# Optimization experiments

Measured on AMD Instinct MI355X. Metric: run time of the kernel, lower is better.

Reference implementation:

```python
import jax, jax.numpy as jnp
import numpy as np

MARGIN = 0.3
EPS = 1e-6  # torch TripletMarginLoss pairwise_distance eps


def setup_inputs() -> dict:
    key = jax.random.key(0)
    k1, k2 = jax.random.split(key)
    n, d = 8192, 128
    inputs = jax.random.normal(k1, (n, d), dtype=jnp.float32)
    similarity = jax.random.randint(k2, (n, n), 0, 2, dtype=jnp.int32)
    return {"inputs": inputs, "similarity": similarity}


def reference(inputs, similarity):
    # mask[i, j] = True if j is a positive of anchor i
    mask = similarity != 0                      # (n, n) bool
    maskf = mask.astype(inputs.dtype)
    counts = maskf.sum(axis=1, keepdims=True)   # (n, 1), >0 by construction
    # per-anchor center = mean of its positives (masked mean as a GEMM)
    centers = (maskf @ inputs) / counts         # (n, d)
    # dist[i, j] = ||centers[i] - inputs[j]||_2 via the expansion trick
    # (avoids materializing the (n, n, d) difference tensor of the original)
    c2 = jnp.sum(centers * centers, axis=1)[:, None]
    x2 = jnp.sum(inputs * inputs, axis=1)[None, :]
    d2 = c2 + x2 - 2.0 * (centers @ inputs.T)
    dist = jnp.sqrt(jnp.maximum(d2, 0.0))       # (n, n)
    # dist only feeds argmin in the original (indices carry no grad)
    dist = jax.lax.stop_gradient(dist)
    # hard-negative mining: argmin of dist over negatives of each anchor
    neg_idx = jnp.argmin(jnp.where(mask, jnp.inf, dist), axis=1)  # (n,)
    neg_min = inputs[neg_idx]                   # (n, d)
    # TripletMarginLoss(margin=0.3, p=2): anchor=centers, pos=inputs, neg=neg_min
    d_ap = jnp.linalg.norm(centers - inputs + EPS, axis=1)
    d_an = jnp.linalg.norm(centers - neg_min + EPS, axis=1)
    return jnp.mean(jnp.maximum(d_ap - d_an + MARGIN, 0.0))
```

## Files before the change

### kernel.cpp

```cpp
#include <hip/hip_runtime.h>
#include <stdint.h>

#define NN 8192
#define DD 128

typedef float f32x4 __attribute__((ext_vector_type(4)));
typedef short bf16x8 __attribute__((ext_vector_type(8)));

union B8 { uint32_t u[4]; bf16x8 v; };

__device__ inline uint16_t f2bf(float f) {
  uint32_t u = __builtin_bit_cast(uint32_t, f);
  uint32_t r = (u + 0x7FFFu + ((u >> 16) & 1u)) >> 16;
  return (uint16_t)r;
}

__device__ inline f32x4 mfma16(bf16x8 a, bf16x8 b, f32x4 c) {
  return __builtin_amdgcn_mfma_f32_16x16x32_bf16(a, b, c, 0, 0, 0);
}

__global__ __launch_bounds__(256) void k_prep(const float* __restrict__ inp,
                                              uint16_t* __restrict__ inp_bf,
                                              uint16_t* __restrict__ inpT_bf,
                                              float* __restrict__ x2p) {
  __shared__ uint16_t ldsT[128 * 65];
  __shared__ float ldsS[256];
  const int tid = threadIdx.x;
  const int j0 = blockIdx.x * 64;
  const int r = tid >> 2;
  const int dseg = (tid & 3) * 32;
  float ss = 0.f;
#pragma unroll
  for (int it = 0; it < 8; ++it) {
    float4 v = *(const float4*)(inp + (size_t)(j0 + r) * DD + dseg + it * 4);
    ss += v.x * v.x + v.y * v.y + v.z * v.z + v.w * v.w;
    uint16_t b0 = f2bf(v.x), b1 = f2bf(v.y), b2 = f2bf(v.z), b3 = f2bf(v.w);
    *(ushort4*)(inp_bf + (size_t)(j0 + r) * DD + dseg + it * 4) = make_ushort4(b0, b1, b2, b3);
    int d = dseg + it * 4;
    ldsT[(d + 0) * 65 + r] = b0;
    ldsT[(d + 1) * 65 + r] = b1;
    ldsT[(d + 2) * 65 + r] = b2;
    ldsT[(d + 3) * 65 + r] = b3;
  }
  ldsS[tid] = ss;
  __syncthreads();
  if (tid < 64)
    x2p[j0 + tid] = ldsS[tid * 4] + ldsS[tid * 4 + 1] + ldsS[tid * 4 + 2] + ldsS[tid * 4 + 3] + 512.0f;
#pragma unroll
  for (int it = 0; it < 32; ++it) {
    int flat = it * 256 + tid;
    int d = flat >> 6, jl = flat & 63;
    inpT_bf[(size_t)d * NN + j0 + jl] = ldsT[d * 65 + jl];
  }
}

__global__ __launch_bounds__(256) void k_bitgen(const int* __restrict__ sim,
                                                uint32_t* __restrict__ bmT,
                                                uint32_t* __restrict__ counts) {
  __shared__ uint32_t ldsW[64 * 64];
  const int tid = threadIdx.x, lane = tid & 63, w = tid >> 6;
  const int m0 = blockIdx.x * 64;
  const int c0 = blockIdx.y * 2048;
#pragma unroll 1
  for (int rr = 0; rr < 16; ++rr) {
    const int rl = rr * 4 + w;
    const int row = m0 + rl;
    const int* p = sim + (size_t)row * NN + c0 + lane;
    int v[32];
#pragma unroll
    for (int s = 0; s < 32; ++s) v[s] = p[s * 64];
    uint32_t cnt = 0;
#pragma unroll
    for (int s = 0; s < 32; ++s) {
      unsigned long long ball = __ballot(v[s] != 0);
      cnt += (uint32_t)__popcll(ball);
      if ((lane & 31) == 0)
        ldsW[(s * 2 + (lane >> 5)) * 64 + rl] = (uint32_t)(ball >> (lane & 32));
    }
    if (lane == 0) atomicAdd(&counts[row], cnt);
  }
  __syncthreads();
#pragma unroll
  for (int it = 0; it < 16; ++it) {
    int idx = it * 256 + tid;
    int kw = idx >> 6, r = idx & 63;
    bmT[(size_t)((c0 >> 5) + kw) * NN + m0 + r] = ldsW[idx];
  }
}

__global__ __launch_bounds__(256, 4) void k_gemm1(const uint16_t* __restrict__ inpT,
                                                  const uint32_t* __restrict__ bmT,
                                                  float* __restrict__ part) {
  __shared__ __align__(16) uint16_t ldsB[128 * 40];
  __shared__ uint32_t ldsM[64];
  const int tid = threadIdx.x, lane = tid & 63, w = tid >> 6;
  const int col = lane & 15, quad = lane >> 4;
  const int m0 = blockIdx.x * 64;
  const int kb0 = blockIdx.y * 1024;
  const int wm = (w >> 1) * 32, wn = (w & 1) * 64;
  const int dim = tid >> 1, koff = (tid & 1) * 16;
  f32x4 acc[2][4];
  const f32x4 z = {0.f, 0.f, 0.f, 0.f};
#pragma unroll
  for (int r = 0; r < 2; ++r)
#pragma unroll
    for (int c = 0; c < 4; ++c) acc[r][c] = z;

  bf16x8 bpf0 = *(const bf16x8*)(inpT + (size_t)dim * NN + kb0 + koff);
  bf16x8 bpf1 = *(const bf16x8*)(inpT + (size_t)dim * NN + kb0 + koff + 8);
  uint32_t mpf = (tid < 64) ? bmT[(size_t)(kb0 >> 5) * NN + m0 + tid] : 0u;

  for (int ks = 0; ks < 32; ++ks) {
    const int kb = kb0 + ks * 32;
    __syncthreads();
    *(bf16x8*)(ldsB + dim * 40 + koff) = bpf0;
    *(bf16x8*)(ldsB + dim * 40 + koff + 8) = bpf1;
    if (tid < 64) ldsM[tid] = mpf;
    __syncthreads();
    if (ks < 31) {
      bpf0 = *(const bf16x8*)(inpT + (size_t)dim * NN + kb + 32 + koff);
      bpf1 = *(const bf16x8*)(inpT + (size_t)dim * NN + kb + 32 + koff + 8);
      if (tid < 64) mpf = bmT[(size_t)((kb + 32) >> 5) * NN + m0 + tid];
    }
    B8 af[2];
#pragma unroll
    for (int rr = 0; rr < 2; ++rr) {
      uint32_t word = ldsM[wm + rr * 16 + col];
      uint32_t b = (word >> (quad * 8)) & 0xFFu;
      uint32_t s = b * 0x8001u;
#pragma unroll
      for (int p = 0; p < 4; ++p) {
        uint32_t t = (s >> (2 * p)) & 0x10001u;
        af[rr].u[p] = t * 0x3F80u;
      }
    }
#pragma unroll
    for (int cc = 0; cc < 4; ++cc) {
      bf16x8 bfr = *(const bf16x8*)(ldsB + (wn + cc * 16 + col) * 40 + quad * 8);
#pragma unroll
      for (int rr = 0; rr < 2; ++rr) acc[rr][cc] = mfma16(af[rr].v, bfr, acc[rr][cc]);
    }
  }
  float* pp = part + (size_t)blockIdx.y * NN * DD;
#pragma unroll
  for (int rr = 0; rr < 2; ++rr)
#pragma unroll
    for (int cc = 0; cc < 4; ++cc)
#pragma unroll
      for (int g = 0; g < 4; ++g)
        pp[(size_t)(m0 + wm + rr * 16 + quad * 4 + g) * DD + wn + cc * 16 + col] = acc[rr][cc][g];
}

__global__ __launch_bounds__(256) void k_reduce(const float* __restrict__ part,
                                                const uint32_t* __restrict__ counts,
                                                float* __restrict__ centers,
                                                uint16_t* __restrict__ cen_bf) {
  const int gid = blockIdx.x * 256 + threadIdx.x;
  const int idx = gid * 4;
  const int row = idx >> 7;
  const float inv = 1.0f / (float)counts[row];
  float4 v = *(const float4*)(part + idx);
#pragma unroll
  for (int s = 1; s < 8; ++s) {
    float4 u = *(const float4*)(part + (size_t)s * NN * DD + idx);
    v.x += u.x; v.y += u.y; v.z += u.z; v.w += u.w;
  }
  v.x *= inv; v.y *= inv; v.z *= inv; v.w *= inv;
  *(float4*)(centers + idx) = v;
  *(ushort4*)(cen_bf + idx) = make_ushort4(f2bf(v.x), f2bf(v.y), f2bf(v.z), f2bf(v.w));
}

__global__ __launch_bounds__(256, 4) void k_argmin(const uint16_t* __restrict__ cen_bf,
                                                   const uint16_t* __restrict__ inp_bf,
                                                   const uint32_t* __restrict__ bmT,
                                                   const float* __restrict__ x2p,
                                                   uint32_t* __restrict__ negkey) {
  __shared__ __align__(16) uint16_t ldsB[64 * 136];
  __shared__ uint32_t ldsM[128];
  __shared__ float ldsX[64];
  __shared__ uint32_t ldsR[64];
  const int tid = threadIdx.x, lane = tid & 63, w = tid >> 6;
  const int col = lane & 15, quad = lane >> 4;
  const int i0 = blockIdx.x * 64;
  const int jbase = blockIdx.y * 1024;
  const int wi = (w >> 1) * 32, wj = (w & 1) * 32;
  bf16x8 af[2][4];
#pragma unroll
  for (int rr = 0; rr < 2; ++rr)
#pragma unroll
    for (int kk = 0; kk < 4; ++kk)
      af[rr][kk] = *(const bf16x8*)(cen_bf + (size_t)(i0 + wi + rr * 16 + col) * DD + kk * 32 + quad * 8);
  if (tid < 64) ldsR[tid] = 0xFFFFFFFFu;
  uint32_t best[2][4];
#pragma unroll
  for (int rr = 0; rr < 2; ++rr)
#pragma unroll
    for (int g = 0; g < 4; ++g) best[rr][g] = 0xFFFFFFFFu;

  const int jl = tid >> 2, doff = (tid & 3) * 32;
  bf16x8 bpf[4];
#pragma unroll
  for (int it = 0; it < 4; ++it)
    bpf[it] = *(const bf16x8*)(inp_bf + (size_t)(jbase + jl) * DD + doff + it * 8);
  uint32_t mpf = (tid < 128) ? bmT[(size_t)((jbase >> 5) + (tid >> 6)) * NN + i0 + (tid & 63)] : 0u;
  float xpf = (tid >= 128 && tid < 192) ? x2p[jbase + tid - 128] : 0.f;

  for (int js = 0; js < 16; ++js) {
    const int j0 = jbase + js * 64;
    __syncthreads();
#pragma unroll
    for (int it = 0; it < 4; ++it)
      *(bf16x8*)(ldsB + jl * 136 + doff + it * 8) = bpf[it];
    if (tid < 128) ldsM[tid] = mpf;
    else if (tid < 192) ldsX[tid - 128] = xpf;
    __syncthreads();
    if (js < 15) {
#pragma unroll
      for (int it = 0; it < 4; ++it)
        bpf[it] = *(const bf16x8*)(inp_bf + (size_t)(j0 + 64 + jl) * DD + doff + it * 8);
      if (tid < 128) mpf = bmT[(size_t)(((j0 + 64) >> 5) + (tid >> 6)) * NN + i0 + (tid & 63)];
      else if (tid < 192) xpf = x2p[j0 + 64 + tid - 128];
    }
    f32x4 acc[2][2];
    const f32x4 z = {0.f, 0.f, 0.f, 0.f};
    acc[0][0] = z; acc[0][1] = z; acc[1][0] = z; acc[1][1] = z;
#pragma unroll
    for (int kk = 0; kk < 4; ++kk) {
      bf16x8 b0 = *(const bf16x8*)(ldsB + (wj + col) * 136 + kk * 32 + quad * 8);
      bf16x8 b1 = *(const bf16x8*)(ldsB + (wj + 16 + col) * 136 + kk * 32 + quad * 8);
      acc[0][0] = mfma16(af[0][kk], b0, acc[0][0]);
      acc[0][1] = mfma16(af[0][kk], b1, acc[0][1]);
      acc[1][0] = mfma16(af[1][kk], b0, acc[1][0]);
      acc[1][1] = mfma16(af[1][kk], b1, acc[1][1]);
    }
    const uint32_t wsel = (w & 1) * 64;
    uint32_t words[2][4];
#pragma unroll
    for (int rr = 0; rr < 2; ++rr)
#pragma unroll
      for (int g = 0; g < 4; ++g) words[rr][g] = ldsM[wsel + wi + rr * 16 + quad * 4 + g];
#pragma unroll
    for (int cc = 0; cc < 2; ++cc) {
      const int jj = wj + cc * 16 + col;
      const float xq = ldsX[jj];
      const uint32_t jpre = (uint32_t)(j0 + jj);
      const int sh = 31 - (cc * 16 + col);
#pragma unroll
      for (int rr = 0; rr < 2; ++rr)
#pragma unroll
        for (int g = 0; g < 4; ++g) {
          float v = fmaf(-2.0f, acc[rr][cc][g], xq);
          uint32_t u = __builtin_bit_cast(uint32_t, v);
          uint32_t key = (u & 0xFFFFE000u) | jpre;
          key |= (words[rr][g] << sh) & 0x80000000u;
          best[rr][g] = min(best[rr][g], key);
        }
    }
  }
#pragma unroll
  for (int rr = 0; rr < 2; ++rr)
#pragma unroll
    for (int g = 0; g < 4; ++g) {
      uint32_t k = best[rr][g];
#pragma unroll
      for (int d = 1; d < 16; d <<= 1) {
        uint32_t o = (uint32_t)__shfl_xor((int)k, d);
        k = min(k, o);
      }
      if (col == 0) atomicMin(&ldsR[wi + rr * 16 + quad * 4 + g], k);
    }
  __syncthreads();
  if (tid < 64) atomicMin(&negkey[i0 + tid], ldsR[tid]);
}

__global__ __launch_bounds__(256) void k_loss(const float* __restrict__ centers,
                                              const float* __restrict__ inp,
                                              const uint32_t* __restrict__ negkey,
                                              float* __restrict__ out) {
  __shared__ float lds[4];
  const int tid = threadIdx.x, lane = tid & 63, w = tid >> 6;
  float local = 0.f;
#pragma unroll 1
  for (int a = 0; a < 4; ++a) {
    int i = blockIdx.x * 16 + w * 4 + a;
    float2 c = *(const float2*)(centers + (size_t)i * DD + lane * 2);
    float2 x = *(const float2*)(inp + (size_t)i * DD + lane * 2);
    uint32_t ni = negkey[i] & (NN - 1);
    float2 gv = *(const float2*)(inp + (size_t)ni * DD + lane * 2);
    float e0 = c.x - x.x + 1e-6f, e1 = c.y - x.y + 1e-6f;
    float f0 = c.x - gv.x + 1e-6f, f1 = c.y - gv.y + 1e-6f;
    float dap = e0 * e0 + e1 * e1;
    float dan = f0 * f0 + f1 * f1;
#pragma unroll
    for (int d = 32; d; d >>= 1) {
      dap += __shfl_down(dap, d);
      dan += __shfl_down(dan, d);
    }
    if (lane == 0) local += fmaxf(sqrtf(dap) - sqrtf(dan) + 0.3f, 0.f);
  }
  if (lane == 0) lds[w] = local;
  __syncthreads();
  if (tid == 0) atomicAdd(out, (lds[0] + lds[1] + lds[2] + lds[3]) * (1.0f / 8192.0f));
}

extern "C" void kernel_launch(void* const* d_in, const int* in_sizes, int n_in,
                              void* d_out, int out_size, void* d_ws, size_t ws_size,
                              hipStream_t stream) {
  (void)in_sizes; (void)n_in; (void)ws_size;
  const float* inp = (const float*)d_in[0];
  const int* sim = (const int*)d_in[1];
  float* out = (float*)d_out;
  char* ws = (char*)d_ws;

  uint32_t* bmT     = (uint32_t*)ws;
  float* part       = (float*)(ws + (8u << 20));
  float* centers    = (float*)(ws + (40u << 20));
  uint16_t* inp_bf  = (uint16_t*)(ws + (44u << 20));
  uint16_t* inpT_bf = (uint16_t*)(ws + (46u << 20));
  uint16_t* cen_bf  = (uint16_t*)(ws + (48u << 20));
  float* x2p        = (float*)(ws + (50u << 20));
  uint32_t* counts  = (uint32_t*)(ws + (50u << 20) + 32768u);
  uint32_t* negkey  = (uint32_t*)(ws + (50u << 20) + 65536u);

  hipMemsetAsync(counts, 0, NN * sizeof(uint32_t), stream);
  hipMemsetAsync(negkey, 0xFF, NN * sizeof(uint32_t), stream);
  hipMemsetAsync(out, 0, out_size * sizeof(float), stream);

  k_prep<<<128, 256, 0, stream>>>(inp, inp_bf, inpT_bf, x2p);
  k_bitgen<<<dim3(128, 4), 256, 0, stream>>>(sim, bmT, counts);
  k_gemm1<<<dim3(128, 8), 256, 0, stream>>>(inpT_bf, bmT, part);
  k_reduce<<<1024, 256, 0, stream>>>(part, counts, centers, cen_bf);
  k_argmin<<<dim3(128, 8), 256, 0, stream>>>(cen_bf, inp_bf, bmT, x2p, negkey);
  k_loss<<<512, 256, 0, stream>>>(centers, inp, negkey, out);
}
```

Baseline: 451.6 us.

## Fuse mask bit generation into masked GEMM and fold memsets into prep kernel

The separate bitmask-generation kernel is removed. The masked-mean GEMM now reads the int similarity matrix directly, builds the per-step 32-bit mask words with wave ballots, accumulates positive counts, and writes the transposed bitmask from LDS for the later argmin kernel. The three memsets are replaced by initialisation stores inside the prep kernel. This removes one kernel launch, three memset launches and a round trip of the bitmask through global memory. In exchange the GEMM main loop carries the heavy similarity-matrix traffic with only one step of prefetch, and its similarity loads are 128-byte row segments rather than full-wave coalesced rows.

```diff
diff --git a/kernel.cpp b/kernel.cpp
--- a/kernel.cpp
+++ b/kernel.cpp
@@ -22,10 +22,16 @@
 __global__ __launch_bounds__(256) void k_prep(const float* __restrict__ inp,
                                               uint16_t* __restrict__ inp_bf,
                                               uint16_t* __restrict__ inpT_bf,
-                                              float* __restrict__ x2p) {
+                                              float* __restrict__ x2p,
+                                              uint32_t* __restrict__ counts,
+                                              uint32_t* __restrict__ negkey,
+                                              float* __restrict__ out) {
   __shared__ uint16_t ldsT[128 * 65];
   __shared__ float ldsS[256];
   const int tid = threadIdx.x;
+  const int gid = blockIdx.x * 256 + tid;
+  if (gid < NN) { counts[gid] = 0u; negkey[gid] = 0xFFFFFFFFu; }
+  if (gid == 0) out[0] = 0.f;
   const int j0 = blockIdx.x * 64;
   const int r = tid >> 2;
   const int dseg = (tid & 3) * 32;
@@ -54,51 +60,23 @@
   }
 }
 
-__global__ __launch_bounds__(256) void k_bitgen(const int* __restrict__ sim,
-                                                uint32_t* __restrict__ bmT,
-                                                uint32_t* __restrict__ counts) {
-  __shared__ uint32_t ldsW[64 * 64];
-  const int tid = threadIdx.x, lane = tid & 63, w = tid >> 6;
-  const int m0 = blockIdx.x * 64;
-  const int c0 = blockIdx.y * 2048;
-#pragma unroll 1
-  for (int rr = 0; rr < 16; ++rr) {
-    const int rl = rr * 4 + w;
-    const int row = m0 + rl;
-    const int* p = sim + (size_t)row * NN + c0 + lane;
-    int v[32];
-#pragma unroll
-    for (int s = 0; s < 32; ++s) v[s] = p[s * 64];
-    uint32_t cnt = 0;
-#pragma unroll
-    for (int s = 0; s < 32; ++s) {
-      unsigned long long ball = __ballot(v[s] != 0);
-      cnt += (uint32_t)__popcll(ball);
-      if ((lane & 31) == 0)
-        ldsW[(s * 2 + (lane >> 5)) * 64 + rl] = (uint32_t)(ball >> (lane & 32));
-    }
-    if (lane == 0) atomicAdd(&counts[row], cnt);
-  }
-  __syncthreads();
-#pragma unroll
-  for (int it = 0; it < 16; ++it) {
-    int idx = it * 256 + tid;
-    int kw = idx >> 6, r = idx & 63;
-    bmT[(size_t)((c0 >> 5) + kw) * NN + m0 + r] = ldsW[idx];
-  }
-}
-
-__global__ __launch_bounds__(256, 4) void k_gemm1(const uint16_t* __restrict__ inpT,
-                                                  const uint32_t* __restrict__ bmT,
-                                                  float* __restrict__ part) {
+__global__ __launch_bounds__(256, 4) void k_maskmm(const int* __restrict__ sim,
+                                                   const uint16_t* __restrict__ inpT,
+                                                   uint32_t* __restrict__ bmT,
+                                                   uint32_t* __restrict__ counts,
+                                                   float* __restrict__ part) {
   __shared__ __align__(16) uint16_t ldsB[128 * 40];
   __shared__ uint32_t ldsM[64];
+  __shared__ uint32_t ldsW[32 * 64];
   const int tid = threadIdx.x, lane = tid & 63, w = tid >> 6;
   const int col = lane & 15, quad = lane >> 4;
   const int m0 = blockIdx.x * 64;
   const int kb0 = blockIdx.y * 1024;
   const int wm = (w >> 1) * 32, wn = (w & 1) * 64;
   const int dim = tid >> 1, koff = (tid & 1) * 16;
+  const int rbase = w * 16 + (lane >> 5);
+  const int scol = lane & 31;
+
   f32x4 acc[2][4];
   const f32x4 z = {0.f, 0.f, 0.f, 0.f};
 #pragma unroll
@@ -108,19 +86,37 @@
 
   bf16x8 bpf0 = *(const bf16x8*)(inpT + (size_t)dim * NN + kb0 + koff);
   bf16x8 bpf1 = *(const bf16x8*)(inpT + (size_t)dim * NN + kb0 + koff + 8);
-  uint32_t mpf = (tid < 64) ? bmT[(size_t)(kb0 >> 5) * NN + m0 + tid] : 0u;
+  int sv[8];
+#pragma unroll
+  for (int i = 0; i < 8; ++i)
+    sv[i] = sim[(size_t)(m0 + rbase + 2 * i) * NN + kb0 + scol];
+  uint32_t cnt[8];
+#pragma unroll
+  for (int i = 0; i < 8; ++i) cnt[i] = 0u;
 
   for (int ks = 0; ks < 32; ++ks) {
     const int kb = kb0 + ks * 32;
     __syncthreads();
     *(bf16x8*)(ldsB + dim * 40 + koff) = bpf0;
     *(bf16x8*)(ldsB + dim * 40 + koff + 8) = bpf1;
-    if (tid < 64) ldsM[tid] = mpf;
+#pragma unroll
+    for (int i = 0; i < 8; ++i) {
+      unsigned long long ball = __ballot(sv[i] != 0);
+      uint32_t word = (uint32_t)(ball >> (lane & 32));
+      if ((lane & 31) == 0) {
+        int rr = rbase + 2 * i;
+        ldsM[rr] = word;
+        ldsW[ks * 64 + rr] = word;
+        cnt[i] += (uint32_t)__popc(word);
+      }
+    }
     __syncthreads();
     if (ks < 31) {
       bpf0 = *(const bf16x8*)(inpT + (size_t)dim * NN + kb + 32 + koff);
       bpf1 = *(const bf16x8*)(inpT + (size_t)dim * NN + kb + 32 + koff + 8);
-      if (tid < 64) mpf = bmT[(size_t)((kb + 32) >> 5) * NN + m0 + tid];
+#pragma unroll
+      for (int i = 0; i < 8; ++i)
+        sv[i] = sim[(size_t)(m0 + rbase + 2 * i) * NN + kb + 32 + scol];
     }
     B8 af[2];
 #pragma unroll
@@ -141,6 +137,11 @@
       for (int rr = 0; rr < 2; ++rr) acc[rr][cc] = mfma16(af[rr].v, bfr, acc[rr][cc]);
     }
   }
+  if ((lane & 31) == 0) {
+#pragma unroll
+    for (int i = 0; i < 8; ++i)
+      atomicAdd(&counts[m0 + rbase + 2 * i], cnt[i]);
+  }
   float* pp = part + (size_t)blockIdx.y * NN * DD;
 #pragma unroll
   for (int rr = 0; rr < 2; ++rr)
@@ -149,6 +150,13 @@
 #pragma unroll
       for (int g = 0; g < 4; ++g)
         pp[(size_t)(m0 + wm + rr * 16 + quad * 4 + g) * DD + wn + cc * 16 + col] = acc[rr][cc][g];
+  __syncthreads();
+#pragma unroll
+  for (int it = 0; it < 8; ++it) {
+    int idx = it * 256 + tid;
+    int kw = idx >> 6, r = idx & 63;
+    bmT[(size_t)((kb0 >> 5) + kw) * NN + m0 + r] = ldsW[idx];
+  }
 }
 
 __global__ __launch_bounds__(256) void k_reduce(const float* __restrict__ part,
@@ -306,7 +314,7 @@
 extern "C" void kernel_launch(void* const* d_in, const int* in_sizes, int n_in,
                               void* d_out, int out_size, void* d_ws, size_t ws_size,
                               hipStream_t stream) {
-  (void)in_sizes; (void)n_in; (void)ws_size;
+  (void)in_sizes; (void)n_in; (void)out_size; (void)ws_size;
   const float* inp = (const float*)d_in[0];
   const int* sim = (const int*)d_in[1];
   float* out = (float*)d_out;
@@ -322,13 +330,8 @@
   uint32_t* counts  = (uint32_t*)(ws + (50u << 20) + 32768u);
   uint32_t* negkey  = (uint32_t*)(ws + (50u << 20) + 65536u);
 
-  hipMemsetAsync(counts, 0, NN * sizeof(uint32_t), stream);
-  hipMemsetAsync(negkey, 0xFF, NN * sizeof(uint32_t), stream);
-  hipMemsetAsync(out, 0, out_size * sizeof(float), stream);
-
-  k_prep<<<128, 256, 0, stream>>>(inp, inp_bf, inpT_bf, x2p);
-  k_bitgen<<<dim3(128, 4), 256, 0, stream>>>(sim, bmT, counts);
-  k_gemm1<<<dim3(128, 8), 256, 0, stream>>>(inpT_bf, bmT, part);
+  k_prep<<<128, 256, 0, stream>>>(inp, inp_bf, inpT_bf, x2p, counts, negkey, out);
+  k_maskmm<<<dim3(128, 8), 256, 0, stream>>>(sim, inpT_bf, bmT, counts, part);
   k_reduce<<<1024, 256, 0, stream>>>(part, counts, centers, cen_bf);
   k_argmin<<<dim3(128, 8), 256, 0, stream>>>(cen_bf, inp_bf, bmT, x2p, negkey);
   k_loss<<<512, 256, 0, stream>>>(centers, inp, negkey, out);
```

Result: slower. 469.0 us (+3.8%).
